# Performance work log

Measured on AMD Instinct MI355X. Metric: run time of the kernel, lower is better.

Reference implementation:

```python
import jax, jax.numpy as jnp
import numpy as np

D_MODEL = 768
N_HEADS = 12
D_K = D_MODEL // N_HEADS


def setup_inputs() -> dict:
    key = jax.random.key(0)
    ks = jax.random.split(key, 9)
    s = 1.0 / np.sqrt(D_MODEL)
    return {
        "x": jax.random.normal(ks[0], (2, 2048, D_MODEL), dtype=jnp.float32),
        "w_q": jax.random.normal(ks[1], (D_MODEL, D_MODEL), dtype=jnp.float32) * s,
        "b_q": jax.random.normal(ks[2], (D_MODEL,), dtype=jnp.float32) * 0.02,
        "w_k": jax.random.normal(ks[3], (D_MODEL, D_MODEL), dtype=jnp.float32) * s,
        "b_k": jax.random.normal(ks[4], (D_MODEL,), dtype=jnp.float32) * 0.02,
        "w_v": jax.random.normal(ks[5], (D_MODEL, D_MODEL), dtype=jnp.float32) * s,
        "b_v": jax.random.normal(ks[6], (D_MODEL,), dtype=jnp.float32) * 0.02,
        "w_o": jax.random.normal(ks[7], (D_MODEL, D_MODEL), dtype=jnp.float32) * s,
        "b_o": jax.random.normal(ks[8], (D_MODEL,), dtype=jnp.float32) * 0.02,
    }


def reference(x, w_q, b_q, w_k, b_k, w_v, b_v, w_o, b_o):
    B, S, _ = x.shape
    # nn.Linear: y = x @ W^T + b
    def proj(w, b):
        y = jnp.einsum("bsd,ed->bse", x, w) + b
        # [B, S, D] -> [B, H, S, d_k]
        return y.reshape(B, S, N_HEADS, D_K).transpose(0, 2, 1, 3)

    q = proj(w_q, b_q)
    k = proj(w_k, b_k)
    v = proj(w_v, b_v)

    scale = 1.0 / np.sqrt(D_K).astype(np.float32)
    scores = jnp.einsum("bhqd,bhkd->bhqk", q, k) * scale  # [B,H,S,S]
    attn = jax.nn.softmax(scores, axis=-1)
    ctx = jnp.einsum("bhqk,bhkd->bhqd", attn, v)  # [B,H,S,d_k]
    ctx = ctx.transpose(0, 2, 1, 3).reshape(B, S, D_MODEL)
    out = jnp.einsum("bsd,ed->bse", ctx, w_o) + b_o
    return out
```

## Files before the change

kernel.cpp:

```cpp
#include <hip/hip_runtime.h>
#include <hip/hip_bf16.h>

#define B_   2
#define S_   2048
#define D_   768
#define H_   12
#define DK_  64
#define R_   (B_*S_)
#define LOG2E_OVER8 0.18033688011112042f

typedef __attribute__((ext_vector_type(8))) short short8;
typedef __attribute__((ext_vector_type(4))) float f32x4;

__device__ __forceinline__ short f2b(float f) {
  union { float f; unsigned u; } x; x.f = f;
  unsigned r = x.u + 0x7fffu + ((x.u >> 16) & 1u);
  return (short)(r >> 16);
}

__device__ __forceinline__ unsigned cvt_pk_bf16(float lo, float hi) {
  unsigned r;
  asm("v_cvt_pk_bf16_f32 %0, %1, %2" : "=v"(r) : "v"(lo), "v"(hi));
  return r;
}

__device__ __forceinline__ void gl_lds16(const short* g, short* l) {
  __builtin_amdgcn_global_load_lds(
      (const __attribute__((address_space(1))) void*)g,
      (__attribute__((address_space(3))) void*)l, 16, 0, 0);
}

__global__ void cvt_kernel(const float* __restrict__ x,
                           const float* __restrict__ wq, const float* __restrict__ wk,
                           const float* __restrict__ wv, const float* __restrict__ wo,
                           short* __restrict__ xb, short* __restrict__ wb) {
  const int XQ = R_ * D_ / 4;
  const int WQ = D_ * D_ / 4;
  int idx = blockIdx.x * blockDim.x + threadIdx.x;
  const float* src; short* dst; int off;
  if (idx < XQ) { src = x; dst = xb; off = idx; }
  else {
    int wi = idx - XQ; int w = wi / WQ; off = wi - w * WQ;
    if      (w == 0) { src = wq; dst = wb; }
    else if (w == 1) { src = wk; dst = wb + D_*D_; }
    else if (w == 2) { src = wv; dst = wb + 2*D_*D_; }
    else             { src = wo; dst = wb + 3*D_*D_; }
  }
  float4 v = ((const float4*)src)[off];
  short4 o;
  o.x = f2b(v.x); o.y = f2b(v.y); o.z = f2b(v.z); o.w = f2b(v.w);
  ((short4*)dst)[off] = o;
}

__launch_bounds__(256)
__global__ void qkv_gemm_kernel(const short* __restrict__ xb, const short* __restrict__ wb,
                                const float* __restrict__ bq, const float* __restrict__ bk,
                                const float* __restrict__ bv,
                                short* __restrict__ Qw, short* __restrict__ Kw,
                                short* __restrict__ VTw) {
  __shared__ short As[2][128 * 32];
  __shared__ short Bs[2][128 * 32];
  const int which = blockIdx.z;
  const short* W = wb + which * (D_ * D_);
  const float* bias = (which == 0) ? bq : (which == 1) ? bk : bv;
  const int n0 = blockIdx.x * 128, m0 = blockIdx.y * 128;
  const int t = threadIdx.x, l = t & 63, w = t >> 6;
  const int wr = w >> 1, wc = w & 1;

  f32x4 acc[4][4] = {};
  const int srow = t >> 2, sseg = (t & 3) * 8;

#define GSTAGE(buf, k0) do { \
    gl_lds16(xb + (m0 + srow) * D_ + (k0) + sseg,      &As[buf][t * 8]); \
    gl_lds16(xb + (m0 + 64 + srow) * D_ + (k0) + sseg, &As[buf][(t + 256) * 8]); \
    gl_lds16(W  + (n0 + srow) * D_ + (k0) + sseg,      &Bs[buf][t * 8]); \
    gl_lds16(W  + (n0 + 64 + srow) * D_ + (k0) + sseg, &Bs[buf][(t + 256) * 8]); \
  } while (0)

  GSTAGE(0, 0);
  __syncthreads();
  int cur = 0;
  for (int k0 = 0; k0 < D_; k0 += 32) {
    if (k0 + 32 < D_) GSTAGE(cur ^ 1, k0 + 32);
    short8 a[4], b[4];
#pragma unroll
    for (int i = 0; i < 4; i++)
      a[i] = *(const short8*)&As[cur][(wr * 64 + i * 16 + (l & 15)) * 32 + (l >> 4) * 8];
#pragma unroll
    for (int i = 0; i < 4; i++)
      b[i] = *(const short8*)&Bs[cur][(wc * 64 + i * 16 + (l & 15)) * 32 + (l >> 4) * 8];
#pragma unroll
    for (int i = 0; i < 4; i++)
#pragma unroll
      for (int j = 0; j < 4; j++)
        acc[i][j] = __builtin_amdgcn_mfma_f32_16x16x32_bf16(a[i], b[j], acc[i][j], 0, 0, 0);
    __syncthreads();
    cur ^= 1;
  }
#undef GSTAGE

#pragma unroll
  for (int i = 0; i < 4; i++) {
#pragma unroll
    for (int j2 = 0; j2 < 4; j2++) {
      int mm = m0 + wr * 64 + i * 16 + (l >> 4) * 4 + j2;
      int bidx = mm >> 11, s = mm & 2047;
#pragma unroll
      for (int nj = 0; nj < 4; nj++) {
        int e = n0 + wc * 64 + nj * 16 + (l & 15);
        float val = acc[i][nj][j2] + bias[e];
        int h = e >> 6, dk = e & 63;
        int bh = bidx * H_ + h;
        if (which == 0)      Qw[(bh * S_ + s) * DK_ + dk] = f2b(val * LOG2E_OVER8);
        else if (which == 1) Kw[(bh * S_ + s) * DK_ + dk] = f2b(val);
        else                 VTw[(bh * DK_ + dk) * S_ + s] = f2b(val);
      }
    }
  }
}

#define KVB   32
#define SHALF 1024
__launch_bounds__(256, 3)
__global__ void attn_kernel(const short* __restrict__ Qw, const short* __restrict__ Kw,
                            const short* __restrict__ VTw, short* __restrict__ ctx) {
  __shared__ short Ksh[2][2][KVB * DK_];
  __shared__ short Vsh[2][2][KVB * DK_];
  __shared__ short Psh[4][32 * 40];

  const int t = threadIdx.x, l = t & 63, w = t >> 6;
  const int s = w >> 1, qh = w & 1;
  const int L = blockIdx.y * 32 + blockIdx.x;
  const int xcd = L & 7, idx = L >> 3;
  const int bh = xcd * 3 + (idx >> 5);
  const int qblk = idx & 31;
  const int q0 = qblk * 64 + qh * 32;
  const int bq = bh / H_, h = bh - bq * H_;
  const short* Qh = Qw + bh * S_ * DK_;
  const short* Kh = Kw + (bh * S_ + s * SHALF) * DK_;
  const short* Vh = VTw + bh * DK_ * S_ + s * SHALF;
  short* pl = &Psh[w][0];

  const int tt = t & 127;
  const int kr0 = tt >> 3, kc0 = tt & 7;
  const int koff0 = kr0 * DK_ + ((kc0 ^ (kr0 & 7)) << 3);
  const int vc8 = (tt & 7) ^ ((tt >> 3) & 7);
  const int vr0 = 2 * (tt >> 3) + (vc8 >> 2);
  const int voff0 = vr0 * S_ + ((vc8 & 3) << 3);

#define STAGE(buf, kt) do { \
    gl_lds16(Kh + (kt) * DK_ + koff0,        &Ksh[s][buf][tt * 8]); \
    gl_lds16(Kh + (kt) * DK_ + koff0 + 1024, &Ksh[s][buf][tt * 8 + 1024]); \
    gl_lds16(Vh + (kt) + voff0,              &Vsh[s][buf][tt * 8]); \
    gl_lds16(Vh + (kt) + voff0 + 32 * S_,    &Vsh[s][buf][tt * 8 + 1024]); \
  } while (0)

  short8 qf[2][2];
#pragma unroll
  for (int mi = 0; mi < 2; mi++)
#pragma unroll
    for (int ks = 0; ks < 2; ks++)
      qf[mi][ks] = *(const short8*)&Qh[(q0 + 16 * mi + (l & 15)) * DK_ + ks * 32 + (l >> 4) * 8];

  f32x4 acc_o[2][4] = {};
  float m_run[2] = {-3.0e38f, -3.0e38f};
  float l_run[2] = {0.f, 0.f};

  STAGE(0, 0);
  __syncthreads();
  int cur = 0;

  for (int kt = 0; kt < SHALF; kt += KVB) {
    if (kt + KVB < SHALF) STAGE(cur ^ 1, kt + KVB);

    f32x4 acc_s[2][2] = {};
    __builtin_amdgcn_s_setprio(1);
#pragma unroll
    for (int ni = 0; ni < 2; ni++) {
      int r = (l & 15) + 16 * ni;
#pragma unroll
      for (int ks = 0; ks < 2; ks++) {
        int cc = (l >> 4) + 4 * ks;
        short8 kf = *(const short8*)&Ksh[s][cur][r * DK_ + ((cc ^ (r & 7)) << 3)];
        acc_s[0][ni] = __builtin_amdgcn_mfma_f32_16x16x32_bf16(kf, qf[0][ks], acc_s[0][ni], 0, 0, 0);
        acc_s[1][ni] = __builtin_amdgcn_mfma_f32_16x16x32_bf16(kf, qf[1][ks], acc_s[1][ni], 0, 0, 0);
      }
    }
    __builtin_amdgcn_s_setprio(0);

    float mx[2];
#pragma unroll
    for (int mi = 0; mi < 2; mi++) {
      float m = -3.0e38f;
#pragma unroll
      for (int ni = 0; ni < 2; ni++)
#pragma unroll
        for (int j = 0; j < 4; j++) m = fmaxf(m, acc_s[mi][ni][j]);
      m = fmaxf(m, __shfl_xor(m, 16));
      m = fmaxf(m, __shfl_xor(m, 32));
      mx[mi] = m;
    }
    float dm = fmaxf(mx[0] - m_run[0], mx[1] - m_run[1]);
    if (!__all(dm <= 11.5f)) {
#pragma unroll
      for (int mi = 0; mi < 2; mi++) {
        float mnew = fmaxf(m_run[mi], mx[mi]);
        float fac = __builtin_amdgcn_exp2f(m_run[mi] - mnew);
        m_run[mi] = mnew;
        l_run[mi] *= fac;
        float fj[4];
#pragma unroll
        for (int j = 0; j < 4; j++) fj[j] = __shfl(fac, ((l >> 4) << 2) + j);
#pragma unroll
        for (int nd = 0; nd < 4; nd++)
#pragma unroll
          for (int j = 0; j < 4; j++) acc_o[mi][nd][j] *= fj[j];
      }
    }
#pragma unroll
    for (int mi = 0; mi < 2; mi++) {
      float sum = 0.f;
#pragma unroll
      for (int ni = 0; ni < 2; ni++)
#pragma unroll
        for (int j = 0; j < 4; j++) {
          float p = __builtin_amdgcn_exp2f(acc_s[mi][ni][j] - m_run[mi]);
          acc_s[mi][ni][j] = p;
          sum += p;
        }
      sum += __shfl_xor(sum, 16);
      sum += __shfl_xor(sum, 32);
      l_run[mi] += sum;
#pragma unroll
      for (int ni = 0; ni < 2; ni++) {
        uint2 pw;
        pw.x = cvt_pk_bf16(acc_s[mi][ni][0], acc_s[mi][ni][1]);
        pw.y = cvt_pk_bf16(acc_s[mi][ni][2], acc_s[mi][ni][3]);
        *(uint2*)&pl[(16 * mi + (l & 15)) * 40 + (l >> 4) * 4 + 16 * ni] = pw;
      }
    }

    __builtin_amdgcn_s_setprio(1);
    {
      short8 pa0 = *(const short8*)&pl[(l & 15) * 40 + (l >> 4) * 8];
      short8 pa1 = *(const short8*)&pl[(16 + (l & 15)) * 40 + (l >> 4) * 8];
#pragma unroll
      for (int nd = 0; nd < 4; nd++) {
        int vr = (l & 15) + 16 * nd, rp = vr >> 1;
        int c8 = ((vr & 1) << 2) + (l >> 4), ph = c8 ^ (rp & 7);
        short8 vf = *(const short8*)&Vsh[s][cur][rp * 64 + (ph << 3)];
        acc_o[0][nd] = __builtin_amdgcn_mfma_f32_16x16x32_bf16(pa0, vf, acc_o[0][nd], 0, 0, 0);
        acc_o[1][nd] = __builtin_amdgcn_mfma_f32_16x16x32_bf16(pa1, vf, acc_o[1][nd], 0, 0, 0);
      }
    }
    __builtin_amdgcn_s_setprio(0);

    __syncthreads();
    cur ^= 1;
  }

  __syncthreads();
  float* Oshf = (float*)&Ksh[0][0][0];
  float* Mshf = (float*)&Vsh[0][0][0];
  if (s == 1) {
#pragma unroll
    for (int mi = 0; mi < 2; mi++)
#pragma unroll
      for (int nd = 0; nd < 4; nd++)
#pragma unroll
        for (int j = 0; j < 4; j++)
          Oshf[qh * 2048 + (16 * mi + (l >> 4) * 4 + j) * 64 + (l & 15) + 16 * nd] = acc_o[mi][nd][j];
    if ((l >> 4) == 0) {
#pragma unroll
      for (int mi = 0; mi < 2; mi++) {
        Mshf[qh * 64 + mi * 32 + l] = m_run[mi];
        Mshf[256 + qh * 64 + mi * 32 + l] = l_run[mi];
      }
    }
  }
  __syncthreads();
  if (s == 0) {
#pragma unroll
    for (int mi = 0; mi < 2; mi++) {
#pragma unroll
      for (int j = 0; j < 4; j++) {
        int src = ((l >> 4) << 2) + j;
        float mlo = __shfl(m_run[mi], src);
        float llo = __shfl(l_run[mi], src);
        float mhi = Mshf[qh * 64 + mi * 32 + src];
        float lhi = Mshf[256 + qh * 64 + mi * 32 + src];
        float mM = fmaxf(mlo, mhi);
        float ea = __builtin_amdgcn_exp2f(mlo - mM);
        float eb = __builtin_amdgcn_exp2f(mhi - mM);
        float inv = 1.f / (llo * ea + lhi * eb);
        int srow = q0 + 16 * mi + src;
#pragma unroll
        for (int nd = 0; nd < 4; nd++) {
          float ohi = Oshf[qh * 2048 + (16 * mi + src) * 64 + (l & 15) + 16 * nd];
          float val = (acc_o[mi][nd][j] * ea + ohi * eb) * inv;
          ctx[(bq * S_ + srow) * D_ + h * DK_ + (l & 15) + 16 * nd] = f2b(val);
        }
      }
    }
  }
#undef STAGE
}

__launch_bounds__(256)
__global__ void oproj_kernel(const short* __restrict__ ctx, const short* __restrict__ Wo,
                             const float* __restrict__ bo, float* __restrict__ out) {
  __shared__ short As[2][128 * 32];
  __shared__ short Bs[2][128 * 32];
  const int n0 = blockIdx.x * 128, m0 = blockIdx.y * 128;
  const int t = threadIdx.x, l = t & 63, w = t >> 6;
  const int wr = w >> 1, wc = w & 1;

  f32x4 acc[4][4] = {};
  const int srow = t >> 2, sseg = (t & 3) * 8;

#define GSTAGE(buf, k0) do { \
    gl_lds16(ctx + (m0 + srow) * D_ + (k0) + sseg,      &As[buf][t * 8]); \
    gl_lds16(ctx + (m0 + 64 + srow) * D_ + (k0) + sseg, &As[buf][(t + 256) * 8]); \
    gl_lds16(Wo  + (n0 + srow) * D_ + (k0) + sseg,      &Bs[buf][t * 8]); \
    gl_lds16(Wo  + (n0 + 64 + srow) * D_ + (k0) + sseg, &Bs[buf][(t + 256) * 8]); \
  } while (0)

  GSTAGE(0, 0);
  __syncthreads();
  int cur = 0;
  for (int k0 = 0; k0 < D_; k0 += 32) {
    if (k0 + 32 < D_) GSTAGE(cur ^ 1, k0 + 32);
    short8 a[4], b[4];
#pragma unroll
    for (int i = 0; i < 4; i++)
      a[i] = *(const short8*)&As[cur][(wr * 64 + i * 16 + (l & 15)) * 32 + (l >> 4) * 8];
#pragma unroll
    for (int i = 0; i < 4; i++)
      b[i] = *(const short8*)&Bs[cur][(wc * 64 + i * 16 + (l & 15)) * 32 + (l >> 4) * 8];
#pragma unroll
    for (int i = 0; i < 4; i++)
#pragma unroll
      for (int j = 0; j < 4; j++)
        acc[i][j] = __builtin_amdgcn_mfma_f32_16x16x32_bf16(a[i], b[j], acc[i][j], 0, 0, 0);
    __syncthreads();
    cur ^= 1;
  }
#undef GSTAGE

#pragma unroll
  for (int i = 0; i < 4; i++) {
#pragma unroll
    for (int j2 = 0; j2 < 4; j2++) {
      int mm = m0 + wr * 64 + i * 16 + (l >> 4) * 4 + j2;
#pragma unroll
      for (int nj = 0; nj < 4; nj++) {
        int e = n0 + wc * 64 + nj * 16 + (l & 15);
        out[mm * D_ + e] = acc[i][nj][j2] + bo[e];
      }
    }
  }
}

extern "C" void kernel_launch(void* const* d_in, const int* in_sizes, int n_in,
                              void* d_out, int out_size, void* d_ws, size_t ws_size,
                              hipStream_t stream) {
  (void)in_sizes; (void)n_in; (void)out_size; (void)ws_size;
  const float* x  = (const float*)d_in[0];
  const float* wq = (const float*)d_in[1];
  const float* bq = (const float*)d_in[2];
  const float* wk = (const float*)d_in[3];
  const float* bk = (const float*)d_in[4];
  const float* wv = (const float*)d_in[5];
  const float* bv = (const float*)d_in[6];
  const float* wo = (const float*)d_in[7];
  const float* bo = (const float*)d_in[8];
  float* out = (float*)d_out;

  short* xb  = (short*)d_ws;
  short* wb  = xb + R_ * D_;
  short* Qw  = wb + 4 * D_ * D_;
  short* Kw  = Qw + R_ * D_;
  short* VTw = Kw + R_ * D_;
  short* ctx = VTw + R_ * D_;

  cvt_kernel<<<5376, 256, 0, stream>>>(x, wq, wk, wv, wo, xb, wb);
  qkv_gemm_kernel<<<dim3(6, 32, 3), 256, 0, stream>>>(xb, wb, bq, bk, bv, Qw, Kw, VTw);
  attn_kernel<<<dim3(32, 24), 256, 0, stream>>>(Qw, Kw, VTw, ctx);
  oproj_kernel<<<dim3(6, 32), 256, 0, stream>>>(ctx, wb + 3 * D_ * D_, bo, out);
}
```

Before: 110.5 us.

## Load K/V fragments straight into registers and keep P in registers

The attention kernel no longer stages K and V tiles through shared memory with a double-buffered async copy and a per-tile barrier. Each wave now loads its K and V MFMA fragments directly from global memory into two register buffers that alternate across iterations. The softmax probabilities are packed into the PV operand in registers, with the key order permuted to match the V load pattern, instead of going through a per-wave LDS scratch. This removes LDS traffic and the __syncthreads in the main loop. In exchange, waves that share K/V read it redundantly from global/L2, the V reads are strided short4 loads with poorer coalescing, and register pressure rises under the 3-blocks-per-SIMD launch bound.

```diff
diff --git a/kernel.cpp b/kernel.cpp
--- a/kernel.cpp
+++ b/kernel.cpp
@@ -124,9 +124,8 @@
 __launch_bounds__(256, 3)
 __global__ void attn_kernel(const short* __restrict__ Qw, const short* __restrict__ Kw,
                             const short* __restrict__ VTw, short* __restrict__ ctx) {
-  __shared__ short Ksh[2][2][KVB * DK_];
-  __shared__ short Vsh[2][2][KVB * DK_];
-  __shared__ short Psh[4][32 * 40];
+  __shared__ float Osh[2][32 * 64];
+  __shared__ float Msh[512];
 
   const int t = threadIdx.x, l = t & 63, w = t >> 6;
   const int s = w >> 1, qh = w & 1;
@@ -139,20 +138,93 @@
   const short* Qh = Qw + bh * S_ * DK_;
   const short* Kh = Kw + (bh * S_ + s * SHALF) * DK_;
   const short* Vh = VTw + bh * DK_ * S_ + s * SHALF;
-  short* pl = &Psh[w][0];
-
-  const int tt = t & 127;
-  const int kr0 = tt >> 3, kc0 = tt & 7;
-  const int koff0 = kr0 * DK_ + ((kc0 ^ (kr0 & 7)) << 3);
-  const int vc8 = (tt & 7) ^ ((tt >> 3) & 7);
-  const int vr0 = 2 * (tt >> 3) + (vc8 >> 2);
-  const int voff0 = vr0 * S_ + ((vc8 & 3) << 3);
-
-#define STAGE(buf, kt) do { \
-    gl_lds16(Kh + (kt) * DK_ + koff0,        &Ksh[s][buf][tt * 8]); \
-    gl_lds16(Kh + (kt) * DK_ + koff0 + 1024, &Ksh[s][buf][tt * 8 + 1024]); \
-    gl_lds16(Vh + (kt) + voff0,              &Vsh[s][buf][tt * 8]); \
-    gl_lds16(Vh + (kt) + voff0 + 32 * S_,    &Vsh[s][buf][tt * 8 + 1024]); \
+
+  union V8 { short4 h[2]; short8 v; };
+
+#define LOADT(KF, VF, kt) do { \
+    _Pragma("unroll") \
+    for (int ni = 0; ni < 2; ni++) \
+      _Pragma("unroll") \
+      for (int ks = 0; ks < 2; ks++) \
+        KF[ni][ks] = *(const short8*)&Kh[((kt) + 16 * ni + (l & 15)) * DK_ + 32 * ks + (l >> 4) * 8]; \
+    _Pragma("unroll") \
+    for (int nd = 0; nd < 4; nd++) { \
+      VF[nd].h[0] = *(const short4*)&Vh[((l & 15) + 16 * nd) * S_ + (kt) + 4 * (l >> 4)]; \
+      VF[nd].h[1] = *(const short4*)&Vh[((l & 15) + 16 * nd) * S_ + (kt) + 16 + 4 * (l >> 4)]; \
+    } \
+  } while (0)
+
+#define COMPUTE(KF, VF) do { \
+    f32x4 acc_s[2][2] = {}; \
+    __builtin_amdgcn_s_setprio(1); \
+    _Pragma("unroll") \
+    for (int ni = 0; ni < 2; ni++) \
+      _Pragma("unroll") \
+      for (int ks = 0; ks < 2; ks++) { \
+        acc_s[0][ni] = __builtin_amdgcn_mfma_f32_16x16x32_bf16(KF[ni][ks], qf[0][ks], acc_s[0][ni], 0, 0, 0); \
+        acc_s[1][ni] = __builtin_amdgcn_mfma_f32_16x16x32_bf16(KF[ni][ks], qf[1][ks], acc_s[1][ni], 0, 0, 0); \
+      } \
+    __builtin_amdgcn_s_setprio(0); \
+    float mx[2]; \
+    _Pragma("unroll") \
+    for (int mi = 0; mi < 2; mi++) { \
+      float m = -3.0e38f; \
+      _Pragma("unroll") \
+      for (int ni = 0; ni < 2; ni++) \
+        _Pragma("unroll") \
+        for (int j = 0; j < 4; j++) m = fmaxf(m, acc_s[mi][ni][j]); \
+      m = fmaxf(m, __shfl_xor(m, 16)); \
+      m = fmaxf(m, __shfl_xor(m, 32)); \
+      mx[mi] = m; \
+    } \
+    float dm = fmaxf(mx[0] - m_run[0], mx[1] - m_run[1]); \
+    if (!__all(dm <= 11.5f)) { \
+      _Pragma("unroll") \
+      for (int mi = 0; mi < 2; mi++) { \
+        float mnew = fmaxf(m_run[mi], mx[mi]); \
+        float fac = __builtin_amdgcn_exp2f(m_run[mi] - mnew); \
+        m_run[mi] = mnew; \
+        l_run[mi] *= fac; \
+        float fj[4]; \
+        _Pragma("unroll") \
+        for (int j = 0; j < 4; j++) fj[j] = __shfl(fac, ((l >> 4) << 2) + j); \
+        _Pragma("unroll") \
+        for (int nd = 0; nd < 4; nd++) \
+          _Pragma("unroll") \
+          for (int j = 0; j < 4; j++) acc_o[mi][nd][j] *= fj[j]; \
+      } \
+    } \
+    union PK { unsigned u[4]; short8 v; } pa0, pa1; \
+    _Pragma("unroll") \
+    for (int mi = 0; mi < 2; mi++) { \
+      float sum = 0.f; \
+      _Pragma("unroll") \
+      for (int ni = 0; ni < 2; ni++) \
+        _Pragma("unroll") \
+        for (int j = 0; j < 4; j++) { \
+          float p = __builtin_amdgcn_exp2f(acc_s[mi][ni][j] - m_run[mi]); \
+          acc_s[mi][ni][j] = p; \
+          sum += p; \
+        } \
+      sum += __shfl_xor(sum, 16); \
+      sum += __shfl_xor(sum, 32); \
+      l_run[mi] += sum; \
+    } \
+    pa0.u[0] = cvt_pk_bf16(acc_s[0][0][0], acc_s[0][0][1]); \
+    pa0.u[1] = cvt_pk_bf16(acc_s[0][0][2], acc_s[0][0][3]); \
+    pa0.u[2] = cvt_pk_bf16(acc_s[0][1][0], acc_s[0][1][1]); \
+    pa0.u[3] = cvt_pk_bf16(acc_s[0][1][2], acc_s[0][1][3]); \
+    pa1.u[0] = cvt_pk_bf16(acc_s[1][0][0], acc_s[1][0][1]); \
+    pa1.u[1] = cvt_pk_bf16(acc_s[1][0][2], acc_s[1][0][3]); \
+    pa1.u[2] = cvt_pk_bf16(acc_s[1][1][0], acc_s[1][1][1]); \
+    pa1.u[3] = cvt_pk_bf16(acc_s[1][1][2], acc_s[1][1][3]); \
+    __builtin_amdgcn_s_setprio(1); \
+    _Pragma("unroll") \
+    for (int nd = 0; nd < 4; nd++) { \
+      acc_o[0][nd] = __builtin_amdgcn_mfma_f32_16x16x32_bf16(pa0.v, VF[nd].v, acc_o[0][nd], 0, 0, 0); \
+      acc_o[1][nd] = __builtin_amdgcn_mfma_f32_16x16x32_bf16(pa1.v, VF[nd].v, acc_o[1][nd], 0, 0, 0); \
+    } \
+    __builtin_amdgcn_s_setprio(0); \
   } while (0)
 
   short8 qf[2][2];
@@ -166,115 +238,31 @@
   float m_run[2] = {-3.0e38f, -3.0e38f};
   float l_run[2] = {0.f, 0.f};
 
-  STAGE(0, 0);
-  __syncthreads();
-  int cur = 0;
-
-  for (int kt = 0; kt < SHALF; kt += KVB) {
-    if (kt + KVB < SHALF) STAGE(cur ^ 1, kt + KVB);
-
-    f32x4 acc_s[2][2] = {};
-    __builtin_amdgcn_s_setprio(1);
-#pragma unroll
-    for (int ni = 0; ni < 2; ni++) {
-      int r = (l & 15) + 16 * ni;
-#pragma unroll
-      for (int ks = 0; ks < 2; ks++) {
-        int cc = (l >> 4) + 4 * ks;
-        short8 kf = *(const short8*)&Ksh[s][cur][r * DK_ + ((cc ^ (r & 7)) << 3)];
-        acc_s[0][ni] = __builtin_amdgcn_mfma_f32_16x16x32_bf16(kf, qf[0][ks], acc_s[0][ni], 0, 0, 0);
-        acc_s[1][ni] = __builtin_amdgcn_mfma_f32_16x16x32_bf16(kf, qf[1][ks], acc_s[1][ni], 0, 0, 0);
-      }
-    }
-    __builtin_amdgcn_s_setprio(0);
-
-    float mx[2];
-#pragma unroll
-    for (int mi = 0; mi < 2; mi++) {
-      float m = -3.0e38f;
-#pragma unroll
-      for (int ni = 0; ni < 2; ni++)
-#pragma unroll
-        for (int j = 0; j < 4; j++) m = fmaxf(m, acc_s[mi][ni][j]);
-      m = fmaxf(m, __shfl_xor(m, 16));
-      m = fmaxf(m, __shfl_xor(m, 32));
-      mx[mi] = m;
-    }
-    float dm = fmaxf(mx[0] - m_run[0], mx[1] - m_run[1]);
-    if (!__all(dm <= 11.5f)) {
+  short8 kfA[2][2], kfB[2][2];
+  V8 vfA[4], vfB[4];
+
+  LOADT(kfA, vfA, 0);
+#pragma unroll 1
+  for (int kt = 0; kt < SHALF; kt += 2 * KVB) {
+    LOADT(kfB, vfB, kt + KVB);
+    COMPUTE(kfA, vfA);
+    if (kt + 2 * KVB < SHALF) LOADT(kfA, vfA, kt + 2 * KVB);
+    COMPUTE(kfB, vfB);
+  }
+
+  if (s == 1) {
+#pragma unroll
+    for (int mi = 0; mi < 2; mi++)
+#pragma unroll
+      for (int nd = 0; nd < 4; nd++)
+#pragma unroll
+        for (int j = 0; j < 4; j++)
+          Osh[qh][(16 * mi + (l >> 4) * 4 + j) * 64 + (l & 15) + 16 * nd] = acc_o[mi][nd][j];
+    if ((l >> 4) == 0) {
 #pragma unroll
       for (int mi = 0; mi < 2; mi++) {
-        float mnew = fmaxf(m_run[mi], mx[mi]);
-        float fac = __builtin_amdgcn_exp2f(m_run[mi] - mnew);
-        m_run[mi] = mnew;
-        l_run[mi] *= fac;
-        float fj[4];
-#pragma unroll
-        for (int j = 0; j < 4; j++) fj[j] = __shfl(fac, ((l >> 4) << 2) + j);
-#pragma unroll
-        for (int nd = 0; nd < 4; nd++)
-#pragma unroll
-          for (int j = 0; j < 4; j++) acc_o[mi][nd][j] *= fj[j];
-      }
-    }
-#pragma unroll
-    for (int mi = 0; mi < 2; mi++) {
-      float sum = 0.f;
-#pragma unroll
-      for (int ni = 0; ni < 2; ni++)
-#pragma unroll
-        for (int j = 0; j < 4; j++) {
-          float p = __builtin_amdgcn_exp2f(acc_s[mi][ni][j] - m_run[mi]);
-          acc_s[mi][ni][j] = p;
-          sum += p;
-        }
-      sum += __shfl_xor(sum, 16);
-      sum += __shfl_xor(sum, 32);
-      l_run[mi] += sum;
-#pragma unroll
-      for (int ni = 0; ni < 2; ni++) {
-        uint2 pw;
-        pw.x = cvt_pk_bf16(acc_s[mi][ni][0], acc_s[mi][ni][1]);
-        pw.y = cvt_pk_bf16(acc_s[mi][ni][2], acc_s[mi][ni][3]);
-        *(uint2*)&pl[(16 * mi + (l & 15)) * 40 + (l >> 4) * 4 + 16 * ni] = pw;
-      }
-    }
-
-    __builtin_amdgcn_s_setprio(1);
-    {
-      short8 pa0 = *(const short8*)&pl[(l & 15) * 40 + (l >> 4) * 8];
-      short8 pa1 = *(const short8*)&pl[(16 + (l & 15)) * 40 + (l >> 4) * 8];
-#pragma unroll
-      for (int nd = 0; nd < 4; nd++) {
-        int vr = (l & 15) + 16 * nd, rp = vr >> 1;
-        int c8 = ((vr & 1) << 2) + (l >> 4), ph = c8 ^ (rp & 7);
-        short8 vf = *(const short8*)&Vsh[s][cur][rp * 64 + (ph << 3)];
-        acc_o[0][nd] = __builtin_amdgcn_mfma_f32_16x16x32_bf16(pa0, vf, acc_o[0][nd], 0, 0, 0);
-        acc_o[1][nd] = __builtin_amdgcn_mfma_f32_16x16x32_bf16(pa1, vf, acc_o[1][nd], 0, 0, 0);
-      }
-    }
-    __builtin_amdgcn_s_setprio(0);
-
-    __syncthreads();
-    cur ^= 1;
-  }
-
-  __syncthreads();
-  float* Oshf = (float*)&Ksh[0][0][0];
-  float* Mshf = (float*)&Vsh[0][0][0];
-  if (s == 1) {
-#pragma unroll
-    for (int mi = 0; mi < 2; mi++)
-#pragma unroll
-      for (int nd = 0; nd < 4; nd++)
-#pragma unroll
-        for (int j = 0; j < 4; j++)
-          Oshf[qh * 2048 + (16 * mi + (l >> 4) * 4 + j) * 64 + (l & 15) + 16 * nd] = acc_o[mi][nd][j];
-    if ((l >> 4) == 0) {
-#pragma unroll
-      for (int mi = 0; mi < 2; mi++) {
-        Mshf[qh * 64 + mi * 32 + l] = m_run[mi];
-        Mshf[256 + qh * 64 + mi * 32 + l] = l_run[mi];
+        Msh[qh * 64 + mi * 32 + l] = m_run[mi];
+        Msh[256 + qh * 64 + mi * 32 + l] = l_run[mi];
       }
     }
   }
@@ -287,8 +275,8 @@
         int src = ((l >> 4) << 2) + j;
         float mlo = __shfl(m_run[mi], src);
         float llo = __shfl(l_run[mi], src);
-        float mhi = Mshf[qh * 64 + mi * 32 + src];
-        float lhi = Mshf[256 + qh * 64 + mi * 32 + src];
+        float mhi = Msh[qh * 64 + mi * 32 + src];
+        float lhi = Msh[256 + qh * 64 + mi * 32 + src];
         float mM = fmaxf(mlo, mhi);
         float ea = __builtin_amdgcn_exp2f(mlo - mM);
         float eb = __builtin_amdgcn_exp2f(mhi - mM);
@@ -296,14 +284,15 @@
         int srow = q0 + 16 * mi + src;
 #pragma unroll
         for (int nd = 0; nd < 4; nd++) {
-          float ohi = Oshf[qh * 2048 + (16 * mi + src) * 64 + (l & 15) + 16 * nd];
+          float ohi = Osh[qh][(16 * mi + src) * 64 + (l & 15) + 16 * nd];
           float val = (acc_o[mi][nd][j] * ea + ohi * eb) * inv;
           ctx[(bq * S_ + srow) * D_ + h * DK_ + (l & 15) + 16 * nd] = f2b(val);
         }
       }
     }
   }
-#undef STAGE
+#undef LOADT
+#undef COMPUTE
 }
 
 __launch_bounds__(256)
```

Result: slower. 191.8 us (+73.6%).

## Halve GEMM M-tile and keep attention P in registers instead of LDS

Applied to the files above, without the earlier changes.

The QKV and output-projection GEMMs move from 128x128 to 64x128 tiles, with each wave owning a 64x32 slice. This doubles the number of blocks so more of the many CUs are filled, at the cost of less operand reuse per block. The attention kernel no longer round-trips the softmax probabilities through a shared-memory scratch buffer; it packs them directly into MFMA A-operand registers. To keep the k-index mapping consistent, the V fragments are now read as two 4-element halves from the swizzled LDS layout.

```diff
diff --git a/kernel.cpp b/kernel.cpp
--- a/kernel.cpp
+++ b/kernel.cpp
@@ -58,21 +58,19 @@
                                 const float* __restrict__ bv,
                                 short* __restrict__ Qw, short* __restrict__ Kw,
                                 short* __restrict__ VTw) {
-  __shared__ short As[2][128 * 32];
+  __shared__ short As[2][64 * 32];
   __shared__ short Bs[2][128 * 32];
   const int which = blockIdx.z;
   const short* W = wb + which * (D_ * D_);
   const float* bias = (which == 0) ? bq : (which == 1) ? bk : bv;
-  const int n0 = blockIdx.x * 128, m0 = blockIdx.y * 128;
+  const int n0 = blockIdx.x * 128, m0 = blockIdx.y * 64;
   const int t = threadIdx.x, l = t & 63, w = t >> 6;
-  const int wr = w >> 1, wc = w & 1;
-
-  f32x4 acc[4][4] = {};
+
+  f32x4 acc[4][2] = {};
   const int srow = t >> 2, sseg = (t & 3) * 8;
 
 #define GSTAGE(buf, k0) do { \
     gl_lds16(xb + (m0 + srow) * D_ + (k0) + sseg,      &As[buf][t * 8]); \
-    gl_lds16(xb + (m0 + 64 + srow) * D_ + (k0) + sseg, &As[buf][(t + 256) * 8]); \
     gl_lds16(W  + (n0 + srow) * D_ + (k0) + sseg,      &Bs[buf][t * 8]); \
     gl_lds16(W  + (n0 + 64 + srow) * D_ + (k0) + sseg, &Bs[buf][(t + 256) * 8]); \
   } while (0)
@@ -82,18 +80,18 @@
   int cur = 0;
   for (int k0 = 0; k0 < D_; k0 += 32) {
     if (k0 + 32 < D_) GSTAGE(cur ^ 1, k0 + 32);
-    short8 a[4], b[4];
+    short8 a[4], b[2];
 #pragma unroll
     for (int i = 0; i < 4; i++)
-      a[i] = *(const short8*)&As[cur][(wr * 64 + i * 16 + (l & 15)) * 32 + (l >> 4) * 8];
+      a[i] = *(const short8*)&As[cur][(i * 16 + (l & 15)) * 32 + (l >> 4) * 8];
+#pragma unroll
+    for (int nj = 0; nj < 2; nj++)
+      b[nj] = *(const short8*)&Bs[cur][(w * 32 + nj * 16 + (l & 15)) * 32 + (l >> 4) * 8];
 #pragma unroll
     for (int i = 0; i < 4; i++)
-      b[i] = *(const short8*)&Bs[cur][(wc * 64 + i * 16 + (l & 15)) * 32 + (l >> 4) * 8];
-#pragma unroll
-    for (int i = 0; i < 4; i++)
-#pragma unroll
-      for (int j = 0; j < 4; j++)
-        acc[i][j] = __builtin_amdgcn_mfma_f32_16x16x32_bf16(a[i], b[j], acc[i][j], 0, 0, 0);
+#pragma unroll
+      for (int nj = 0; nj < 2; nj++)
+        acc[i][nj] = __builtin_amdgcn_mfma_f32_16x16x32_bf16(a[i], b[nj], acc[i][nj], 0, 0, 0);
     __syncthreads();
     cur ^= 1;
   }
@@ -103,11 +101,11 @@
   for (int i = 0; i < 4; i++) {
 #pragma unroll
     for (int j2 = 0; j2 < 4; j2++) {
-      int mm = m0 + wr * 64 + i * 16 + (l >> 4) * 4 + j2;
+      int mm = m0 + i * 16 + (l >> 4) * 4 + j2;
       int bidx = mm >> 11, s = mm & 2047;
 #pragma unroll
-      for (int nj = 0; nj < 4; nj++) {
-        int e = n0 + wc * 64 + nj * 16 + (l & 15);
+      for (int nj = 0; nj < 2; nj++) {
+        int e = n0 + w * 32 + nj * 16 + (l & 15);
         float val = acc[i][nj][j2] + bias[e];
         int h = e >> 6, dk = e & 63;
         int bh = bidx * H_ + h;
@@ -126,7 +124,6 @@
                             const short* __restrict__ VTw, short* __restrict__ ctx) {
   __shared__ short Ksh[2][2][KVB * DK_];
   __shared__ short Vsh[2][2][KVB * DK_];
-  __shared__ short Psh[4][32 * 40];
 
   const int t = threadIdx.x, l = t & 63, w = t >> 6;
   const int s = w >> 1, qh = w & 1;
@@ -139,7 +136,6 @@
   const short* Qh = Qw + bh * S_ * DK_;
   const short* Kh = Kw + (bh * S_ + s * SHALF) * DK_;
   const short* Vh = VTw + bh * DK_ * S_ + s * SHALF;
-  short* pl = &Psh[w][0];
 
   const int tt = t & 127;
   const int kr0 = tt >> 3, kc0 = tt & 7;
@@ -231,26 +227,32 @@
       sum += __shfl_xor(sum, 16);
       sum += __shfl_xor(sum, 32);
       l_run[mi] += sum;
-#pragma unroll
-      for (int ni = 0; ni < 2; ni++) {
-        uint2 pw;
-        pw.x = cvt_pk_bf16(acc_s[mi][ni][0], acc_s[mi][ni][1]);
-        pw.y = cvt_pk_bf16(acc_s[mi][ni][2], acc_s[mi][ni][3]);
-        *(uint2*)&pl[(16 * mi + (l & 15)) * 40 + (l >> 4) * 4 + 16 * ni] = pw;
-      }
-    }
+    }
+
+    union PK { unsigned u[4]; short8 v; } pa0, pa1;
+    pa0.u[0] = cvt_pk_bf16(acc_s[0][0][0], acc_s[0][0][1]);
+    pa0.u[1] = cvt_pk_bf16(acc_s[0][0][2], acc_s[0][0][3]);
+    pa0.u[2] = cvt_pk_bf16(acc_s[0][1][0], acc_s[0][1][1]);
+    pa0.u[3] = cvt_pk_bf16(acc_s[0][1][2], acc_s[0][1][3]);
+    pa1.u[0] = cvt_pk_bf16(acc_s[1][0][0], acc_s[1][0][1]);
+    pa1.u[1] = cvt_pk_bf16(acc_s[1][0][2], acc_s[1][0][3]);
+    pa1.u[2] = cvt_pk_bf16(acc_s[1][1][0], acc_s[1][1][1]);
+    pa1.u[3] = cvt_pk_bf16(acc_s[1][1][2], acc_s[1][1][3]);
 
     __builtin_amdgcn_s_setprio(1);
     {
-      short8 pa0 = *(const short8*)&pl[(l & 15) * 40 + (l >> 4) * 8];
-      short8 pa1 = *(const short8*)&pl[(16 + (l & 15)) * 40 + (l >> 4) * 8];
+      const int cc = l >> 4;
+      union V8 { short4 h[2]; short8 v; };
 #pragma unroll
       for (int nd = 0; nd < 4; nd++) {
         int vr = (l & 15) + 16 * nd, rp = vr >> 1;
-        int c8 = ((vr & 1) << 2) + (l >> 4), ph = c8 ^ (rp & 7);
-        short8 vf = *(const short8*)&Vsh[s][cur][rp * 64 + (ph << 3)];
-        acc_o[0][nd] = __builtin_amdgcn_mfma_f32_16x16x32_bf16(pa0, vf, acc_o[0][nd], 0, 0, 0);
-        acc_o[1][nd] = __builtin_amdgcn_mfma_f32_16x16x32_bf16(pa1, vf, acc_o[1][nd], 0, 0, 0);
+        int ph0 = (((vr & 1) << 2) | (cc >> 1)) ^ (rp & 7);
+        int ph1 = (((vr & 1) << 2) | (2 + (cc >> 1))) ^ (rp & 7);
+        V8 vf;
+        vf.h[0] = *(const short4*)&Vsh[s][cur][rp * 64 + ph0 * 8 + (cc & 1) * 4];
+        vf.h[1] = *(const short4*)&Vsh[s][cur][rp * 64 + ph1 * 8 + (cc & 1) * 4];
+        acc_o[0][nd] = __builtin_amdgcn_mfma_f32_16x16x32_bf16(pa0.v, vf.v, acc_o[0][nd], 0, 0, 0);
+        acc_o[1][nd] = __builtin_amdgcn_mfma_f32_16x16x32_bf16(pa1.v, vf.v, acc_o[1][nd], 0, 0, 0);
       }
     }
     __builtin_amdgcn_s_setprio(0);
@@ -309,18 +311,16 @@
 __launch_bounds__(256)
 __global__ void oproj_kernel(const short* __restrict__ ctx, const short* __restrict__ Wo,
                              const float* __restrict__ bo, float* __restrict__ out) {
-  __shared__ short As[2][128 * 32];
+  __shared__ short As[2][64 * 32];
   __shared__ short Bs[2][128 * 32];
-  const int n0 = blockIdx.x * 128, m0 = blockIdx.y * 128;
+  const int n0 = blockIdx.x * 128, m0 = blockIdx.y * 64;
   const int t = threadIdx.x, l = t & 63, w = t >> 6;
-  const int wr = w >> 1, wc = w & 1;
-
-  f32x4 acc[4][4] = {};
+
+  f32x4 acc[4][2] = {};
   const int srow = t >> 2, sseg = (t & 3) * 8;
 
 #define GSTAGE(buf, k0) do { \
     gl_lds16(ctx + (m0 + srow) * D_ + (k0) + sseg,      &As[buf][t * 8]); \
-    gl_lds16(ctx + (m0 + 64 + srow) * D_ + (k0) + sseg, &As[buf][(t + 256) * 8]); \
     gl_lds16(Wo  + (n0 + srow) * D_ + (k0) + sseg,      &Bs[buf][t * 8]); \
     gl_lds16(Wo  + (n0 + 64 + srow) * D_ + (k0) + sseg, &Bs[buf][(t + 256) * 8]); \
   } while (0)
@@ -330,18 +330,18 @@
   int cur = 0;
   for (int k0 = 0; k0 < D_; k0 += 32) {
     if (k0 + 32 < D_) GSTAGE(cur ^ 1, k0 + 32);
-    short8 a[4], b[4];
+    short8 a[4], b[2];
 #pragma unroll
     for (int i = 0; i < 4; i++)
-      a[i] = *(const short8*)&As[cur][(wr * 64 + i * 16 + (l & 15)) * 32 + (l >> 4) * 8];
+      a[i] = *(const short8*)&As[cur][(i * 16 + (l & 15)) * 32 + (l >> 4) * 8];
+#pragma unroll
+    for (int nj = 0; nj < 2; nj++)
+      b[nj] = *(const short8*)&Bs[cur][(w * 32 + nj * 16 + (l & 15)) * 32 + (l >> 4) * 8];
 #pragma unroll
     for (int i = 0; i < 4; i++)
-      b[i] = *(const short8*)&Bs[cur][(wc * 64 + i * 16 + (l & 15)) * 32 + (l >> 4) * 8];
-#pragma unroll
-    for (int i = 0; i < 4; i++)
-#pragma unroll
-      for (int j = 0; j < 4; j++)
-        acc[i][j] = __builtin_amdgcn_mfma_f32_16x16x32_bf16(a[i], b[j], acc[i][j], 0, 0, 0);
+#pragma unroll
+      for (int nj = 0; nj < 2; nj++)
+        acc[i][nj] = __builtin_amdgcn_mfma_f32_16x16x32_bf16(a[i], b[nj], acc[i][nj], 0, 0, 0);
     __syncthreads();
     cur ^= 1;
   }
@@ -351,10 +351,10 @@
   for (int i = 0; i < 4; i++) {
 #pragma unroll
     for (int j2 = 0; j2 < 4; j2++) {
-      int mm = m0 + wr * 64 + i * 16 + (l >> 4) * 4 + j2;
-#pragma unroll
-      for (int nj = 0; nj < 4; nj++) {
-        int e = n0 + wc * 64 + nj * 16 + (l & 15);
+      int mm = m0 + i * 16 + (l >> 4) * 4 + j2;
+#pragma unroll
+      for (int nj = 0; nj < 2; nj++) {
+        int e = n0 + w * 32 + nj * 16 + (l & 15);
         out[mm * D_ + e] = acc[i][nj][j2] + bo[e];
       }
     }
@@ -384,7 +384,7 @@
   short* ctx = VTw + R_ * D_;
 
   cvt_kernel<<<5376, 256, 0, stream>>>(x, wq, wk, wv, wo, xb, wb);
-  qkv_gemm_kernel<<<dim3(6, 32, 3), 256, 0, stream>>>(xb, wb, bq, bk, bv, Qw, Kw, VTw);
+  qkv_gemm_kernel<<<dim3(6, 64, 3), 256, 0, stream>>>(xb, wb, bq, bk, bv, Qw, Kw, VTw);
   attn_kernel<<<dim3(32, 24), 256, 0, stream>>>(Qw, Kw, VTw, ctx);
-  oproj_kernel<<<dim3(6, 32), 256, 0, stream>>>(ctx, wb + 3 * D_ * D_, bo, out);
-}
+  oproj_kernel<<<dim3(6, 64), 256, 0, stream>>>(ctx, wb + 3 * D_ * D_, bo, out);
+}
```

Result: no change. 111.3 us (+0.7%).
